# Kernel tuning notes

Measured on AMD Instinct MI355X. Metric: run time of the kernel, lower is better.

## Reference

```python
import jax, jax.numpy as jnp
import numpy as np

ENC_DIM, DEC_DIM, ATT_DIM = 512, 512, 512
B, S = 32, 4096


def setup_inputs() -> dict:
    key = jax.random.key(0)
    ks = jax.random.split(key, 8)
    sc = lambda d: 1.0 / np.sqrt(d)
    return {
        "input": jax.random.normal(ks[0], (B, S, ENC_DIM), dtype=jnp.float32),
        "dec_h": jax.random.normal(ks[1], (B, DEC_DIM), dtype=jnp.float32),
        "W_enc": jax.random.uniform(ks[2], (ENC_DIM, ATT_DIM), jnp.float32, -sc(ENC_DIM), sc(ENC_DIM)),
        "b_enc": jax.random.uniform(ks[3], (ATT_DIM,), jnp.float32, -sc(ENC_DIM), sc(ENC_DIM)),
        "W_dec": jax.random.uniform(ks[4], (DEC_DIM, ATT_DIM), jnp.float32, -sc(DEC_DIM), sc(DEC_DIM)),
        "b_dec": jax.random.uniform(ks[5], (ATT_DIM,), jnp.float32, -sc(DEC_DIM), sc(DEC_DIM)),
        "w_att": jax.random.uniform(ks[6], (ATT_DIM, 1), jnp.float32, -sc(ATT_DIM), sc(ATT_DIM)),
        "b_att": jax.random.uniform(ks[7], (1,), jnp.float32, -sc(ATT_DIM), sc(ATT_DIM)),
    }


def reference(input, dec_h, W_enc, b_enc, W_dec, b_dec, w_att, b_att):
    # enc_att: [B,S,A]; dec_att: [B,A] broadcast over S
    enc_att = jnp.einsum("bse,ea->bsa", input, W_enc) + b_enc
    dec_att = dec_h @ W_dec + b_dec
    # score: [B,S]
    att = jax.nn.relu(enc_att + dec_att[:, None, :]) @ w_att + b_att  # [B,S,1]
    prob = jax.nn.softmax(att, axis=1)  # softmax over sequence dim
    weighted = jnp.sum(input * prob, axis=1)  # [B,enc_dim]
    return weighted, prob[..., 0]
```

## Files before the change

### kernel.cpp

```cpp
#include <hip/hip_runtime.h>
#include <hip/hip_bf16.h>

typedef __attribute__((ext_vector_type(4))) float f32x4;
typedef __attribute__((ext_vector_type(8))) __bf16 bf16x8;
typedef __attribute__((ext_vector_type(4))) unsigned int u32x4;


__device__ __forceinline__ float lo_bf(unsigned int u) {
  return __builtin_bit_cast(float, u << 16);
}
__device__ __forceinline__ float hi_bf(unsigned int u) {
  return __builtin_bit_cast(float, u & 0xffff0000u);
}

__device__ __forceinline__ void barrier_lgkm() {
  asm volatile("s_waitcnt lgkmcnt(0)" ::: "memory");
  __builtin_amdgcn_s_barrier();
  asm volatile("" ::: "memory");
}

__global__ void prep_w(const float* __restrict__ W_enc, unsigned short* __restrict__ Wf) {
  int idx = blockIdx.x * 256 + threadIdx.x;
  int lane = idx & 63;
  int grp = idx >> 6;
  int nt = grp >> 4, kb = grp & 15;
  int n = nt * 16 + (lane & 15);
  int k0 = kb * 32 + (lane >> 4) * 8;
  unsigned short* dst = Wf + idx * 8;
  #pragma unroll
  for (int j = 0; j < 8; ++j) {
    float f = W_enc[(k0 + j) * 512 + n];
    dst[j] = __builtin_bit_cast(unsigned short, (__bf16)f);
  }
}

__global__ void prep_c(const float* __restrict__ dec_h, const float* __restrict__ W_dec,
                       const float* __restrict__ b_dec, const float* __restrict__ b_enc,
                       float* __restrict__ cpart) {
  int b = blockIdx.x >> 2, j = blockIdx.x & 3;
  int a = threadIdx.x;
  const float* dh = dec_h + b * 512 + j * 128;
  const float* wd = W_dec + (j * 128) * 512 + a;
  float s = (j == 0) ? (b_dec[a] + b_enc[a]) : 0.f;
  #pragma unroll 8
  for (int k = 0; k < 128; ++k) s += dh[k] * wd[k * 512];
  cpart[j * 16384 + b * 512 + a] = s;
}

__global__ __launch_bounds__(1024, 4) void attn_main(
    const float* __restrict__ input, const unsigned short* __restrict__ Wf,
    const float* __restrict__ cpart, const float* __restrict__ w_att,
    float* __restrict__ att_out, float* __restrict__ m_out, float* __restrict__ pw_out) {
  __shared__ u32x4 A4[8192];
  __shared__ float c_lds[512];
  __shared__ float w_lds[512];
  __shared__ float red[8][64];

  char* Al = (char*)A4;
  const int tid = threadIdx.x;
  const int wave = tid >> 6, lane = tid & 63;
  const int l15 = lane & 15, l4 = lane >> 4;
  const int blk = blockIdx.x;
  const int ci0 = blk * 8;
  const int b = ci0 >> 6;
  const bool is_stage = wave >= 8;
  const int st = tid & 511;

  float4 g[4][2];

  auto STAGE_HALF = [&](int ci, int bufsel, int half) {
    const float* base = input + (long)ci * 32768;
    char* dst = Al + bufsel * 65536;
    #pragma unroll
    for (int j = 0; j < 4; ++j) {
      int ch = st + j * 512;
      int row = (ch >> 6) + half * 32, c32 = ch & 63;
      const float4* s4 = (const float4*)(base + row * 512 + c32 * 8);
      g[j][0] = s4[0];
      g[j][1] = s4[1];
    }
    #pragma unroll
    for (int j = 0; j < 4; ++j) {
      int ch = st + j * 512;
      int row = (ch >> 6) + half * 32, c32 = ch & 63;
      bf16x8 v;
      v[0] = (__bf16)g[j][0].x; v[1] = (__bf16)g[j][0].y;
      v[2] = (__bf16)g[j][0].z; v[3] = (__bf16)g[j][0].w;
      v[4] = (__bf16)g[j][1].x; v[5] = (__bf16)g[j][1].y;
      v[6] = (__bf16)g[j][1].z; v[7] = (__bf16)g[j][1].w;
      *(bf16x8*)(dst + row * 1024 + ((c32 * 16) ^ ((row & 7) << 4))) = v;
    }
  };

  if (!is_stage) {
    c_lds[tid] = cpart[b * 512 + tid] + cpart[16384 + b * 512 + tid]
               + cpart[32768 + b * 512 + tid] + cpart[49152 + b * 512 + tid];
    w_lds[tid] = w_att[tid];
  } else {
    STAGE_HALF(ci0, 0, 0);
    STAGE_HALF(ci0, 0, 1);
  }
  barrier_lgkm();

  const bf16x8* Wfp = (const bf16x8*)Wf;

  for (int i = 0; i < 8; ++i) {
    const int ci = ci0 + i;
    const char* Ab = Al + (i & 1) * 65536;
    float p = 0.f;

    if (!is_stage) {
      f32x4 acc[4][4];
      #pragma unroll
      for (int mi = 0; mi < 4; ++mi)
        #pragma unroll
        for (int nj = 0; nj < 4; ++nj) {
          f32x4 z = {0.f, 0.f, 0.f, 0.f};
          acc[mi][nj] = z;
        }
      const bf16x8* wb = Wfp + (wave * 64) * 64 + lane;
      #pragma unroll 2
      for (int kb = 0; kb < 16; ++kb) {
        bf16x8 bv[4];
        #pragma unroll
        for (int nj = 0; nj < 4; ++nj)
          bv[nj] = wb[(nj * 16 + kb) * 64];
        __builtin_amdgcn_s_setprio(1);
        #pragma unroll
        for (int mi = 0; mi < 4; ++mi) {
          int row = mi * 16 + l15;
          bf16x8 afr = *(const bf16x8*)(Ab + row * 1024 + (((kb * 64) + l4 * 16) ^ ((row & 7) << 4)));
          #pragma unroll
          for (int nj = 0; nj < 4; ++nj)
            acc[mi][nj] = __builtin_amdgcn_mfma_f32_16x16x32_bf16(afr, bv[nj], acc[mi][nj], 0, 0, 0);
        }
        __builtin_amdgcn_s_setprio(0);
      }
      float attp[16];
      #pragma unroll
      for (int q = 0; q < 16; ++q) attp[q] = 0.f;
      #pragma unroll
      for (int nj = 0; nj < 4; ++nj) {
        int n = (wave * 4 + nj) * 16 + l15;
        float cc = c_lds[n], ww = w_lds[n];
        #pragma unroll
        for (int mi = 0; mi < 4; ++mi)
          #pragma unroll
          for (int r = 0; r < 4; ++r)
            attp[mi * 4 + r] += fmaxf(acc[mi][nj][r] + cc, 0.f) * ww;
      }
      #pragma unroll
      for (int off = 1; off < 16; off <<= 1)
        #pragma unroll
        for (int q = 0; q < 16; ++q)
          attp[q] += __shfl_xor(attp[q], off, 64);
      if (l15 == 0) {
        #pragma unroll
        for (int mi = 0; mi < 4; ++mi)
          #pragma unroll
          for (int r = 0; r < 4; ++r)
            red[wave][mi * 16 + l4 * 4 + r] = attp[mi * 4 + r];
      }
    } else if (i < 7) {
      STAGE_HALF(ci + 1, (i + 1) & 1, 0);
    }
    barrier_lgkm();

    if (!is_stage) {
      float av = 0.f;
      #pragma unroll
      for (int cw = 0; cw < 8; ++cw) av += red[cw][lane];
      float m = av;
      #pragma unroll
      for (int off = 32; off >= 1; off >>= 1) m = fmaxf(m, __shfl_xor(m, off, 64));
      p = expf(av - m);
      if (wave == 0) {
        att_out[b * 4096 + (ci & 63) * 64 + lane] = av;
        if (lane == 0) m_out[ci] = m;
      }
      const int ub = (tid >> 1) * 4;
      const bool hi = tid & 1;
      float pwa = 0.f;
      #pragma unroll 8
      for (int s = 0; s < 64; ++s) {
        float ps = __shfl(p, s, 64);
        unsigned int u = *(const unsigned int*)(Ab + s * 1024 + (ub ^ ((s & 7) << 4)));
        pwa += ps * (hi ? hi_bf(u) : lo_bf(u));
      }
      pw_out[ci * 512 + tid] = pwa;
    } else if (i < 7) {
      STAGE_HALF(ci + 1, (i + 1) & 1, 1);
    }
    barrier_lgkm();
  }
}

__global__ void finalize(const float* __restrict__ att, const float* __restrict__ m_blk,
                         const float* __restrict__ pw, float* __restrict__ out) {
  const int bg = blockIdx.x;
  const int b = bg >> 2, g = bg & 3;
  const int tid = threadIdx.x;
  const int wave = tid >> 6, lane = tid & 63;
  __shared__ float wred[4];
  __shared__ float zred[4];
  __shared__ float fac[64];

  float v[16];
  float mx = -3.4e38f;
  #pragma unroll
  for (int i = 0; i < 16; ++i) {
    v[i] = att[b * 4096 + i * 256 + tid];
    mx = fmaxf(mx, v[i]);
  }
  #pragma unroll
  for (int off = 32; off >= 1; off >>= 1) mx = fmaxf(mx, __shfl_xor(mx, off, 64));
  if (lane == 0) wred[wave] = mx;
  __syncthreads();
  mx = fmaxf(fmaxf(wred[0], wred[1]), fmaxf(wred[2], wred[3]));

  float z = 0.f;
  #pragma unroll
  for (int i = 0; i < 16; ++i) { v[i] = expf(v[i] - mx); z += v[i]; }
  #pragma unroll
  for (int off = 32; off >= 1; off >>= 1) z += __shfl_xor(z, off, 64);
  if (lane == 0) zred[wave] = z;
  __syncthreads();
  z = zred[0] + zred[1] + zred[2] + zred[3];
  float invZ = 1.f / z;

  #pragma unroll
  for (int i = 0; i < 4; ++i) {
    int ii = g * 4 + i;
    out[16384 + b * 4096 + ii * 256 + tid] = v[ii] * invZ;
  }

  if (tid < 64) fac[tid] = expf(m_blk[b * 64 + tid] - mx) * invZ;
  __syncthreads();

  int col = g * 128 + (tid >> 1);
  int h = tid & 1;
  float w0 = 0.f;
  #pragma unroll 8
  for (int s = h * 32; s < h * 32 + 32; ++s)
    w0 += fac[s] * pw[(b * 64 + s) * 512 + col];
  w0 += __shfl_xor(w0, 1, 64);
  if (h == 0) out[b * 512 + col] = w0;
}

extern "C" void kernel_launch(void* const* d_in, const int* in_sizes, int n_in,
                              void* d_out, int out_size, void* d_ws, size_t ws_size,
                              hipStream_t stream) {
  const float* input = (const float*)d_in[0];
  const float* dec_h = (const float*)d_in[1];
  const float* W_enc = (const float*)d_in[2];
  const float* b_enc = (const float*)d_in[3];
  const float* W_dec = (const float*)d_in[4];
  const float* b_dec = (const float*)d_in[5];
  const float* w_att = (const float*)d_in[6];
  float* out = (float*)d_out;

  char* ws = (char*)d_ws;
  unsigned short* Wf = (unsigned short*)(ws);
  float* cpart = (float*)(ws + 524288);
  float* att   = (float*)(ws + 786432);
  float* m_b   = (float*)(ws + 1310720);
  float* pw    = (float*)(ws + 1318912);

  hipLaunchKernelGGL(prep_w, dim3(128), dim3(256), 0, stream, W_enc, Wf);
  hipLaunchKernelGGL(prep_c, dim3(128), dim3(512), 0, stream, dec_h, W_dec, b_dec, b_enc, cpart);
  hipLaunchKernelGGL(attn_main, dim3(256), dim3(1024), 0, stream, input, Wf, cpart, w_att, att, m_b, pw);
  hipLaunchKernelGGL(finalize, dim3(128), dim3(256), 0, stream, att, m_b, pw, out);
}
```

Baseline: 129.0 us.

## Transpose MFMA operands and split weighted-sum over sequence rows across waves

Swaps the MFMA operand roles so W is the A operand and the input tile is B, with prep_w's packing reordered to match. The score reduction then needs only two cross-lane shuffles per accumulator instead of sixteen-way butterflies. The p-weighted sum now has each wave read 16-byte vectors for 8 sequence rows across all 512 columns, followed by an extra LDS reduction over waves. This trades narrow per-row LDS reads for wide vector reads at the cost of an additional barrier and shared buffer per chunk.

```diff
diff --git a/kernel.cpp b/kernel.cpp
--- a/kernel.cpp
+++ b/kernel.cpp
@@ -22,9 +22,9 @@
 __global__ void prep_w(const float* __restrict__ W_enc, unsigned short* __restrict__ Wf) {
   int idx = blockIdx.x * 256 + threadIdx.x;
   int lane = idx & 63;
-  int grp = idx >> 6;
-  int nt = grp >> 4, kb = grp & 15;
-  int n = nt * 16 + (lane & 15);
+  int g = idx >> 6;
+  int nt = g & 3, kb = (g >> 2) & 15, w = g >> 6;
+  int n = (w * 4 + nt) * 16 + (lane & 15);
   int k0 = kb * 32 + (lane >> 4) * 8;
   unsigned short* dst = Wf + idx * 8;
   #pragma unroll
@@ -55,6 +55,7 @@
   __shared__ float c_lds[512];
   __shared__ float w_lds[512];
   __shared__ float red[8][64];
+  __shared__ float red2[8 * 8 * 72];
 
   char* Al = (char*)A4;
   const int tid = threadIdx.x;
@@ -64,7 +65,7 @@
   const int ci0 = blk * 8;
   const int b = ci0 >> 6;
   const bool is_stage = wave >= 8;
-  const int st = tid & 511;
+  const int st_id = tid & 511;
 
   float4 g[4][2];
 
@@ -73,7 +74,7 @@
     char* dst = Al + bufsel * 65536;
     #pragma unroll
     for (int j = 0; j < 4; ++j) {
-      int ch = st + j * 512;
+      int ch = st_id + j * 512;
       int row = (ch >> 6) + half * 32, c32 = ch & 63;
       const float4* s4 = (const float4*)(base + row * 512 + c32 * 8);
       g[j][0] = s4[0];
@@ -81,7 +82,7 @@
     }
     #pragma unroll
     for (int j = 0; j < 4; ++j) {
-      int ch = st + j * 512;
+      int ch = st_id + j * 512;
       int row = (ch >> 6) + half * 32, c32 = ch & 63;
       bf16x8 v;
       v[0] = (__bf16)g[j][0].x; v[1] = (__bf16)g[j][0].y;
@@ -107,59 +108,55 @@
   for (int i = 0; i < 8; ++i) {
     const int ci = ci0 + i;
     const char* Ab = Al + (i & 1) * 65536;
-    float p = 0.f;
 
     if (!is_stage) {
       f32x4 acc[4][4];
       #pragma unroll
-      for (int mi = 0; mi < 4; ++mi)
-        #pragma unroll
-        for (int nj = 0; nj < 4; ++nj) {
+      for (int nt = 0; nt < 4; ++nt)
+        #pragma unroll
+        for (int st = 0; st < 4; ++st) {
           f32x4 z = {0.f, 0.f, 0.f, 0.f};
-          acc[mi][nj] = z;
+          acc[nt][st] = z;
         }
       const bf16x8* wb = Wfp + (wave * 64) * 64 + lane;
       #pragma unroll 2
       for (int kb = 0; kb < 16; ++kb) {
-        bf16x8 bv[4];
-        #pragma unroll
-        for (int nj = 0; nj < 4; ++nj)
-          bv[nj] = wb[(nj * 16 + kb) * 64];
+        bf16x8 av4[4];
+        #pragma unroll
+        for (int nt = 0; nt < 4; ++nt)
+          av4[nt] = wb[(kb * 4 + nt) * 64];
         __builtin_amdgcn_s_setprio(1);
         #pragma unroll
-        for (int mi = 0; mi < 4; ++mi) {
-          int row = mi * 16 + l15;
-          bf16x8 afr = *(const bf16x8*)(Ab + row * 1024 + (((kb * 64) + l4 * 16) ^ ((row & 7) << 4)));
+        for (int st = 0; st < 4; ++st) {
+          int row = st * 16 + l15;
+          bf16x8 xf = *(const bf16x8*)(Ab + row * 1024 + (((kb * 64) + l4 * 16) ^ ((row & 7) << 4)));
           #pragma unroll
-          for (int nj = 0; nj < 4; ++nj)
-            acc[mi][nj] = __builtin_amdgcn_mfma_f32_16x16x32_bf16(afr, bv[nj], acc[mi][nj], 0, 0, 0);
+          for (int nt = 0; nt < 4; ++nt)
+            acc[nt][st] = __builtin_amdgcn_mfma_f32_16x16x32_bf16(av4[nt], xf, acc[nt][st], 0, 0, 0);
         }
         __builtin_amdgcn_s_setprio(0);
       }
-      float attp[16];
-      #pragma unroll
-      for (int q = 0; q < 16; ++q) attp[q] = 0.f;
-      #pragma unroll
-      for (int nj = 0; nj < 4; ++nj) {
-        int n = (wave * 4 + nj) * 16 + l15;
-        float cc = c_lds[n], ww = w_lds[n];
-        #pragma unroll
-        for (int mi = 0; mi < 4; ++mi)
+      float attp[4] = {0.f, 0.f, 0.f, 0.f};
+      #pragma unroll
+      for (int nt = 0; nt < 4; ++nt) {
+        #pragma unroll
+        for (int r = 0; r < 4; ++r) {
+          int n = (wave * 4 + nt) * 16 + l4 * 4 + r;
+          float cc = c_lds[n], ww = w_lds[n];
           #pragma unroll
-          for (int r = 0; r < 4; ++r)
-            attp[mi * 4 + r] += fmaxf(acc[mi][nj][r] + cc, 0.f) * ww;
-      }
-      #pragma unroll
-      for (int off = 1; off < 16; off <<= 1)
-        #pragma unroll
-        for (int q = 0; q < 16; ++q)
-          attp[q] += __shfl_xor(attp[q], off, 64);
-      if (l15 == 0) {
-        #pragma unroll
-        for (int mi = 0; mi < 4; ++mi)
-          #pragma unroll
-          for (int r = 0; r < 4; ++r)
-            red[wave][mi * 16 + l4 * 4 + r] = attp[mi * 4 + r];
+          for (int st = 0; st < 4; ++st)
+            attp[st] += fmaxf(acc[nt][st][r] + cc, 0.f) * ww;
+        }
+      }
+      #pragma unroll
+      for (int st = 0; st < 4; ++st) {
+        attp[st] += __shfl_xor(attp[st], 16, 64);
+        attp[st] += __shfl_xor(attp[st], 32, 64);
+      }
+      if (l4 == 0) {
+        #pragma unroll
+        for (int st = 0; st < 4; ++st)
+          red[wave][st * 16 + l15] = attp[st];
       }
     } else if (i < 7) {
       STAGE_HALF(ci + 1, (i + 1) & 1, 0);
@@ -173,23 +170,36 @@
       float m = av;
       #pragma unroll
       for (int off = 32; off >= 1; off >>= 1) m = fmaxf(m, __shfl_xor(m, off, 64));
-      p = expf(av - m);
+      float p = expf(av - m);
       if (wave == 0) {
         att_out[b * 4096 + (ci & 63) * 64 + lane] = av;
         if (lane == 0) m_out[ci] = m;
       }
-      const int ub = (tid >> 1) * 4;
-      const bool hi = tid & 1;
-      float pwa = 0.f;
-      #pragma unroll 8
-      for (int s = 0; s < 64; ++s) {
+      float acc8[8] = {0.f, 0.f, 0.f, 0.f, 0.f, 0.f, 0.f, 0.f};
+      #pragma unroll
+      for (int j = 0; j < 8; ++j) {
+        int s = wave * 8 + j;
         float ps = __shfl(p, s, 64);
-        unsigned int u = *(const unsigned int*)(Ab + s * 1024 + (ub ^ ((s & 7) << 4)));
-        pwa += ps * (hi ? hi_bf(u) : lo_bf(u));
-      }
-      pw_out[ci * 512 + tid] = pwa;
+        u32x4 u = *(const u32x4*)(Ab + s * 1024 + ((lane * 16) ^ ((s & 7) << 4)));
+        acc8[0] += ps * lo_bf(u[0]); acc8[1] += ps * hi_bf(u[0]);
+        acc8[2] += ps * lo_bf(u[1]); acc8[3] += ps * hi_bf(u[1]);
+        acc8[4] += ps * lo_bf(u[2]); acc8[5] += ps * hi_bf(u[2]);
+        acc8[6] += ps * lo_bf(u[3]); acc8[7] += ps * hi_bf(u[3]);
+      }
+      #pragma unroll
+      for (int q = 0; q < 8; ++q)
+        red2[(wave * 8 + q) * 72 + lane] = acc8[q];
     } else if (i < 7) {
       STAGE_HALF(ci + 1, (i + 1) & 1, 1);
+    }
+    barrier_lgkm();
+
+    if (tid < 512) {
+      int lw = tid >> 3, q = tid & 7;
+      float s = 0.f;
+      #pragma unroll
+      for (int w = 0; w < 8; ++w) s += red2[(w * 8 + q) * 72 + lw];
+      pw_out[ci * 512 + lw * 8 + q] = s;
     }
     barrier_lgkm();
   }
```

Result: faster. 113.9 us (-11.7%).
